# Optimization experiments

Measured on AMD Instinct MI355X. Metric: run time of the kernel, lower is better.

## Reference

```python
import jax, jax.numpy as jnp
import numpy as np

MS = 0.001
TAU = 50.0
THRESHOLD = 1.0


def setup_inputs() -> dict:
    key = jax.random.key(0)
    kx, kw = jax.random.split(key)
    x = jax.random.normal(kx, (32, 1024, 1000), dtype=jnp.float32)
    # nn.init.normal_(w, mean=0.0, std=8000)
    w = jax.random.normal(kw, (1024, 1024), dtype=jnp.float32) * 8000.0
    return {"x": x, "w": w}


def reference(x, w):
    # x: [B, n_in, T], w: [n_in, n_out]
    # Precompute all input currents in one batched GEMM: [T, B, n_out]
    currents = jnp.einsum('bit,io->tbo', x, w)

    def step(v, cur):
        v = v + (-v + cur) * (MS / TAU)
        spikes = (v >= THRESHOLD).astype(v.dtype)
        v = v * (1.0 - spikes)
        return v, spikes

    v0 = jnp.zeros((x.shape[0], w.shape[1]), dtype=x.dtype)
    _, out = jax.lax.scan(step, v0, currents)  # out: [T, B, n_out]
    return jnp.transpose(out, (1, 2, 0))  # [B, n_out, T]
```

## Files before the change

kernel.cpp:

```cpp
#include <hip/hip_runtime.h>


#define NB 32
#define NI 1024
#define NO 1024
#define NT 1000
#define NS 5
#define BT 64
#define BO 64
#define KI 32
#define NKB (NI/KI)
#define TILEB (NS*2*64*16)

typedef int i32x4  __attribute__((ext_vector_type(4)));
typedef int i32x16 __attribute__((ext_vector_type(16)));

typedef const __attribute__((address_space(1))) void GVOID;
typedef __attribute__((address_space(3))) void LVOID;
#define GLDS16(g, l) __builtin_amdgcn_global_load_lds((GVOID*)(g), (LVOID*)(l), 16, 0, 0)

__global__ void snn_wscale(const float* __restrict__ w, float* __restrict__ sb)
{
    __shared__ float red[4][64];
    const int tid = threadIdx.x;
    const int ol = tid & 63, iq = tid >> 6;
    const int o = blockIdx.x * 64 + ol;
    float m = 0.f;
    for (int i = iq; i < NI; i += 4) m = fmaxf(m, fabsf(w[(size_t)i * NO + o]));
    red[iq][ol] = m;
    __syncthreads();
    if (iq == 0) {
        m = fmaxf(fmaxf(red[0][ol], red[1][ol]), fmaxf(red[2][ol], red[3][ol]));
        const int e = (__float_as_uint(m) >> 23) & 255;
        float S = 0.f, Si = 0.f;
        if (e) {
            S  = __uint_as_float((unsigned)(e + 1) << 23);
            Si = __uint_as_float((unsigned)(253 - e) << 23);
        }
        sb[o] = S;
        sb[NO + o] = Si;
    }
}

__global__ void snn_wslice(const float* __restrict__ w, const float* __restrict__ sb,
                           signed char* __restrict__ wp)
{
    __shared__ int sldw[NS][64][16];
    const int tid = threadIdx.x;
    const int ol = tid & 63, iq = tid >> 6;
    const int o0 = blockIdx.x * 64, ic = blockIdx.y * 64;
    const float inv = sb[NO + o0 + ol];
#pragma unroll
    for (int q4 = 0; q4 < 16; q4 += 4) {
        int pk[NS] = {0, 0, 0, 0, 0};
#pragma unroll
        for (int j = 0; j < 4; ++j) {
            const int i = ic + iq * 16 + q4 + j;
            float wv = w[(size_t)i * NO + o0 + ol] * inv;
#pragma unroll
            for (int s = 0; s < NS; ++s) {
                const float f = wv * 128.f;
                const int a = (int)f;
                wv = f - (float)a;
                pk[s] |= (a & 255) << (8 * j);
            }
        }
        const int cdw = (iq * 16 + q4) >> 2;
#pragma unroll
        for (int s = 0; s < NS; ++s) sldw[s][ol][cdw ^ (ol & 15)] = pk[s];
    }
    __syncthreads();
    signed char* tb = wp + (size_t)blockIdx.x * (NKB * TILEB) + (size_t)(ic >> 5) * TILEB;
#pragma unroll
    for (int p = 0; p < 20; ++p) {
        const int idx = p * 256 + tid;
        const int kbi = idx >= 2560;
        const int ld  = idx - (kbi ? 2560 : 0);
        const int s  = ld >> 9;
        const int kc = (ld >> 8) & 1;
        const int r  = (ld >> 2) & 63;
        const int d4 = ld & 3;
        *(int*)&tb[(size_t)kbi * TILEB + (size_t)ld * 4] =
            sldw[s][r][(kbi * 8 + kc * 4 + d4) ^ (r & 15)];
    }
}

__global__ void snn_xscale(const float* __restrict__ x, float* __restrict__ sa,
                           int t0, int tca)
{
    __shared__ float red[4][64];
    const int tid = threadIdx.x;
    const int tl = tid & 63, iq = tid >> 6;
    const int b = blockIdx.y;
    const int tt = blockIdx.x * 64;
    const int tg = t0 + tt + tl;
    const float* xb = x + (size_t)b * NI * NT;
    float m = 0.f;
    if (tg < NT)
        for (int i = iq; i < NI; i += 4) m = fmaxf(m, fabsf(xb[(size_t)i * NT + tg]));
    red[iq][tl] = m;
    __syncthreads();
    if (iq == 0) {
        m = fmaxf(fmaxf(red[0][tl], red[1][tl]), fmaxf(red[2][tl], red[3][tl]));
        const int e = (__float_as_uint(m) >> 23) & 255;
        sa[(size_t)b * tca + tt + tl] = e ? __uint_as_float((unsigned)(e + 1) << 23) : 0.f;
    }
}

__global__ void snn_xslice(const float* __restrict__ x, const float* __restrict__ sa,
                           signed char* __restrict__ xp, int t0, int tca, int ntiles)
{
    __shared__ int sldw[NS][64][16];
    const int tid = threadIdx.x;
    const int tl = tid & 63, iq = tid >> 6;
    const int b = blockIdx.y;
    const int tile = blockIdx.x;
    const int tg = t0 + tile * 64 + tl;
    const bool valid = (tg < NT);
    const float* xb = x + (size_t)b * NI * NT;
    const float S = sa[(size_t)b * tca + tile * 64 + tl];
    const float inv = (S > 0.f)
        ? __uint_as_float((254u - (__float_as_uint(S) >> 23)) << 23) : 0.f;
    signed char* tb = xp + (size_t)(b * ntiles + tile) * (NKB * TILEB);

    for (int c4 = 0; c4 < 4; ++c4) {
        const int ic = blockIdx.z * 256 + c4 * 64;
#pragma unroll
        for (int q4 = 0; q4 < 16; q4 += 4) {
            int pk[NS] = {0, 0, 0, 0, 0};
#pragma unroll
            for (int j = 0; j < 4; ++j) {
                const int i = ic + iq * 16 + q4 + j;
                float wv = valid ? xb[(size_t)i * NT + tg] * inv : 0.f;
#pragma unroll
                for (int s = 0; s < NS; ++s) {
                    const float f = wv * 128.f;
                    const int a = (int)f;
                    wv = f - (float)a;
                    pk[s] |= (a & 255) << (8 * j);
                }
            }
            const int cdw = (iq * 16 + q4) >> 2;
#pragma unroll
            for (int s = 0; s < NS; ++s) sldw[s][tl][cdw ^ (tl & 15)] = pk[s];
        }
        __syncthreads();
        signed char* kbb = tb + (size_t)(ic >> 5) * TILEB;
#pragma unroll
        for (int p = 0; p < 20; ++p) {
            const int idx = p * 256 + tid;
            const int kbi = idx >= 2560;
            const int ld  = idx - (kbi ? 2560 : 0);
            const int s  = ld >> 9;
            const int kc = (ld >> 8) & 1;
            const int r  = (ld >> 2) & 63;
            const int d4 = ld & 3;
            *(int*)&kbb[(size_t)kbi * TILEB + (size_t)ld * 4] =
                sldw[s][r][(kbi * 8 + kc * 4 + d4) ^ (r & 15)];
        }
        __syncthreads();
    }
}

__global__ __launch_bounds__(256, 4)
void snn_gemm_i8(const signed char* __restrict__ xp, const signed char* __restrict__ wp,
                 const float* __restrict__ sa, const float* __restrict__ sb,
                 double* __restrict__ cur, int t0, int tca, int ntiles)
{
    __shared__ signed char As[2][TILEB];
    __shared__ signed char Bs[2][TILEB];

    const int tid  = threadIdx.x;
    const int lane = tid & 63;
    const int wave = tid >> 6;
    const int wm = (wave >> 1) * 32;
    const int wn = (wave & 1) * 32;
    const int l31 = lane & 31;
    const int hi  = lane >> 5;

    int lid = blockIdx.x + (int)gridDim.x * (blockIdx.y + (int)gridDim.y * blockIdx.z);
    {
        const int nwg = (int)(gridDim.x * gridDim.y * gridDim.z);
        const int q = nwg >> 3, r = nwg & 7;
        const int xcd = lid & 7, off = lid >> 3;
        lid = (xcd < r ? xcd * (q + 1) : r * (q + 1) + (xcd - r) * q) + off;
    }
    const int ox  = lid & 15;
    const int rst = lid >> 4;
    const int ty  = rst % ntiles;
    const int b   = rst / ntiles;

    const int o0 = ox * BO;
    const int bt = ty * BT;

    i32x16 acc[NS];
#pragma unroll
    for (int c = 0; c < NS; ++c) acc[c] = (i32x16)0;

    const signed char* AgL = xp + (size_t)(b * ntiles + ty) * (NKB * TILEB) + lane * 16;
    const signed char* BgL = wp + (size_t)ox * (NKB * TILEB) + lane * 16;

#define STAGE(src, bsel) do {                                                  \
    if (wave < 2) {                                                            \
        _Pragma("unroll")                                                      \
        for (int u = 0; u < 5; ++u) {                                          \
            const int ck = wave * 5 + u;                                       \
            GLDS16(AgL + (size_t)(src) * TILEB + ck * 1024,                    \
                   &As[bsel][0] + ck * 1024);                                  \
        }                                                                      \
    } else {                                                                   \
        _Pragma("unroll")                                                      \
        for (int u = 0; u < 5; ++u) {                                          \
            const int ck = (wave - 2) * 5 + u;                                 \
            GLDS16(BgL + (size_t)(src) * TILEB + ck * 1024,                    \
                   &Bs[bsel][0] + ck * 1024);                                  \
        }                                                                      \
    } } while (0)

    const int abase = hi * 1024 + (wm + l31) * 16;
    const int bbase = hi * 1024 + (wn + l31) * 16;

#define KITER(slot) do {                                                       \
    const signed char* Ab_ = &As[slot][0];                                     \
    const signed char* Bb_ = &Bs[slot][0];                                     \
    i32x4 bf[NS];                                                              \
    _Pragma("unroll")                                                          \
    for (int s = 0; s < NS; ++s) bf[s] = *(const i32x4*)&Bb_[bbase + s * 2048];\
    i32x4 a0 = *(const i32x4*)&Ab_[abase];                                     \
    _Pragma("unroll")                                                          \
    for (int i = 0; i < NS; ++i) {                                             \
        i32x4 a1 = a0;                                                         \
        if (i + 1 < NS) a1 = *(const i32x4*)&Ab_[abase + (i + 1) * 2048];      \
        __builtin_amdgcn_s_setprio(1);                                         \
        _Pragma("unroll")                                                      \
        for (int c = NS - 1; c >= i; --c)                                      \
            acc[c] = __builtin_amdgcn_mfma_i32_32x32x32_i8(a0, bf[c - i],      \
                                                           acc[c], 0, 0, 0);   \
        __builtin_amdgcn_s_setprio(0);                                         \
        a0 = a1;                                                               \
    } } while (0)

    STAGE(0, 0);
    asm volatile("s_waitcnt vmcnt(0)" ::: "memory");
    __builtin_amdgcn_s_barrier();

    for (int kb = 0; kb < NKB - 1; ++kb) {
        STAGE(kb + 1, (kb + 1) & 1);
        KITER(kb & 1);
        asm volatile("s_waitcnt vmcnt(0)" ::: "memory");
        asm volatile("s_waitcnt lgkmcnt(0)" ::: "memory");
        __builtin_amdgcn_sched_barrier(0);
        __builtin_amdgcn_s_barrier();
    }
    KITER((NKB - 1) & 1);
#undef STAGE
#undef KITER

    int prow[16];
    {
        i32x4 pa, pb;
#pragma unroll
        for (int q = 0; q < 4; ++q) {
            int va = 0, vb = 0;
#pragma unroll
            for (int jj = 0; jj < 4; ++jj) {
                const int k = 16 * hi + q * 4 + jj;
                if (l31 == k) va |= 1 << (8 * jj);
                vb |= (k & 255) << (8 * jj);
            }
            pa[q] = va; pb[q] = vb;
        }
        i32x16 pp = (i32x16)0;
        pp = __builtin_amdgcn_mfma_i32_32x32x32_i8(pa, pb, pp, 0, 0, 0);
#pragma unroll
        for (int r = 0; r < 16; ++r) prow[r] = pp[r] & 31;
    }

    const double c128[NS] = {0x1p-14, 0x1p-21, 0x1p-28, 0x1p-35, 0x1p-42};
    const int ocol = o0 + wn + l31;
    const double sbv = (double)sb[ocol];
#pragma unroll
    for (int r = 0; r < 16; ++r) {
        const int trow = bt + wm + prow[r];
        double v = 0.0;
#pragma unroll
        for (int c = 0; c < NS; ++c) v += (double)acc[c][r] * c128[c];
        v *= (double)sa[(size_t)b * tca + trow] * sbv;
        if (t0 + trow < NT)
            cur[((size_t)trow * NB + b) * NO + ocol] = v;
    }
}

#define NC 32
__global__ __launch_bounds__(64)
void snn_scan_f64(const double* __restrict__ cur, float* __restrict__ out,
                  double* __restrict__ vstate, int t0, int len)
{
    const int gid = blockIdx.x * 64 + threadIdx.x;
    const double dt = 0.001 / 50.0;

    double v = (t0 == 0) ? 0.0 : vstate[gid];
    const double* cp = cur + gid;
    float* op = out + (size_t)gid * NT + t0;

    const size_t ts = (size_t)NB * NO;
    const int nb = len / NC;
    const int rem = len - nb * NC;

    double A[NC], B[NC];
#pragma unroll
    for (int j = 0; j < NC; ++j) A[j] = (j < len) ? cp[(size_t)j * ts] : 0.0;

    for (int blk = 0; blk < nb; ++blk) {
        const int next = (blk + 1) * NC;
#pragma unroll
        for (int j = 0; j < NC; ++j)
            B[j] = (next + j < len) ? cp[(size_t)(next + j) * ts] : 0.0;

#pragma unroll
        for (int q = 0; q < NC; q += 8) {
            float s[8];
#pragma unroll
            for (int j = 0; j < 8; ++j) {
                v = v + (A[q + j] - v) * dt;
                const bool sp = (v >= 1.0);
                s[j] = sp ? 1.0f : 0.0f;
                if (sp) v = 0.0;
            }
            *(float4*)(op + q)     = make_float4(s[0], s[1], s[2], s[3]);
            *(float4*)(op + q + 4) = make_float4(s[4], s[5], s[6], s[7]);
        }
        op += NC;
#pragma unroll
        for (int j = 0; j < NC; ++j) A[j] = B[j];
    }

    for (int q = 0; q < rem; q += 8) {
        float s[8];
#pragma unroll
        for (int j = 0; j < 8; ++j) {
            v = v + (A[q + j] - v) * dt;
            const bool sp = (v >= 1.0);
            s[j] = sp ? 1.0f : 0.0f;
            if (sp) v = 0.0;
        }
        *(float4*)(op + q)     = make_float4(s[0], s[1], s[2], s[3]);
        *(float4*)(op + q + 4) = make_float4(s[4], s[5], s[6], s[7]);
    }
    vstate[gid] = v;
}

extern "C" void kernel_launch(void* const* d_in, const int* in_sizes, int n_in,
                              void* d_out, int out_size, void* d_ws, size_t ws_size,
                              hipStream_t stream)
{
    const float* x = (const float*)d_in[0];
    const float* w = (const float*)d_in[1];
    float* out = (float*)d_out;

    char* p = (char*)d_ws;
    double* vstate = (double*)p;         p += (size_t)NB * NO * 8;
    float* sbv = (float*)p;              p += (size_t)2 * NO * 4;
    signed char* wp = (signed char*)p;   p += (size_t)(NO / 64) * NKB * TILEB;

    const size_t fixed = (size_t)(p - (char*)d_ws);
    const size_t per_t = (size_t)NB * 4
                       + (size_t)NS * NB * NI
                       + (size_t)NB * NO * 8;
    int tca = 512;
    while (tca > 64 && fixed + (size_t)tca * per_t > ws_size) tca -= 64;

    float* sa = (float*)p;               p += (size_t)NB * tca * 4;
    signed char* xpl = (signed char*)p;  p += (size_t)NB * (tca / 64) * NKB * TILEB;
    double* cur = (double*)p;

    snn_wscale<<<dim3(NO / 64), dim3(256), 0, stream>>>(w, sbv);
    snn_wslice<<<dim3(NO / 64, NI / 64), dim3(256), 0, stream>>>(w, sbv, wp);

    for (int t0 = 0; t0 < NT; t0 += tca) {
        const int len = (NT - t0 < tca) ? (NT - t0) : tca;
        const int ntiles = (len + BT - 1) / BT;
        snn_xscale<<<dim3(ntiles, NB), dim3(256), 0, stream>>>(x, sa, t0, tca);
        snn_xslice<<<dim3(ntiles, NB, 4), dim3(256), 0, stream>>>(x, sa, xpl, t0, tca, ntiles);
        snn_gemm_i8<<<dim3(NO / BO, ntiles, NB), dim3(256), 0, stream>>>(
            xpl, wp, sa, sbv, cur, t0, tca, ntiles);
        snn_scan_f64<<<dim3((NB * NO) / 64), dim3(64), 0, stream>>>(
            cur, out, vstate, t0, len);
    }
}
```

Measured before the change: 1.061 ms.

## Load A fragments directly to registers and triple-buffer B in LDS

The int8 GEMM no longer stages the A tile through shared memory. Each wave loads its A fragments from global memory straight into registers, using two alternating register sets. B stays in LDS, now with three buffers and a counted vmcnt wait, so loads can run further ahead of the MFMA work. This removes the LDS traffic and space for A and deepens the pipeline, but it costs more VGPRs, which is why launch bounds drop to 3 waves per SIMD, and the A global loads are duplicated across waves.

Result: no change. 1.072 ms (+1.1%).

```diff
diff --git a/kernel.cpp b/kernel.cpp
--- a/kernel.cpp
+++ b/kernel.cpp
@@ -162,13 +162,12 @@
     }
 }
 
-__global__ __launch_bounds__(256, 4)
+__global__ __launch_bounds__(256, 3)
 void snn_gemm_i8(const signed char* __restrict__ xp, const signed char* __restrict__ wp,
                  const float* __restrict__ sa, const float* __restrict__ sb,
                  double* __restrict__ cur, int t0, int tca, int ntiles)
 {
-    __shared__ signed char As[2][TILEB];
-    __shared__ signed char Bs[2][TILEB];
+    __shared__ signed char Bs[3][TILEB];
 
     const int tid  = threadIdx.x;
     const int lane = tid & 63;
@@ -197,64 +196,69 @@
 #pragma unroll
     for (int c = 0; c < NS; ++c) acc[c] = (i32x16)0;
 
-    const signed char* AgL = xp + (size_t)(b * ntiles + ty) * (NKB * TILEB) + lane * 16;
-    const signed char* BgL = wp + (size_t)ox * (NKB * TILEB) + lane * 16;
-
-#define STAGE(src, bsel) do {                                                  \
-    if (wave < 2) {                                                            \
-        _Pragma("unroll")                                                      \
-        for (int u = 0; u < 5; ++u) {                                          \
-            const int ck = wave * 5 + u;                                       \
-            GLDS16(AgL + (size_t)(src) * TILEB + ck * 1024,                    \
-                   &As[bsel][0] + ck * 1024);                                  \
-        }                                                                      \
-    } else {                                                                   \
-        _Pragma("unroll")                                                      \
-        for (int u = 0; u < 5; ++u) {                                          \
-            const int ck = (wave - 2) * 5 + u;                                 \
-            GLDS16(BgL + (size_t)(src) * TILEB + ck * 1024,                    \
-                   &Bs[bsel][0] + ck * 1024);                                  \
-        }                                                                      \
+    const signed char* Ag = xp + (size_t)(b * ntiles + ty) * (NKB * TILEB)
+                               + hi * 1024 + (wm + l31) * 16;
+    const signed char* Bg = wp + (size_t)ox * (NKB * TILEB) + lane * 16;
+    const int bbase = hi * 1024 + (wn + l31) * 16;
+
+#define ISSUE(src, aset, slot) do {                                            \
+    const signed char* As_ = Ag + (size_t)(src) * TILEB;                       \
+    _Pragma("unroll")                                                          \
+    for (int s = 0; s < NS; ++s)                                               \
+        aset[s] = *(const i32x4*)(As_ + s * 2048);                             \
+    const signed char* Bsrc_ = Bg + (size_t)(src) * TILEB;                     \
+    _Pragma("unroll")                                                          \
+    for (int u = 0; u < 3; ++u) {                                              \
+        int ck = 3 * wave + u; if (ck >= 10) ck -= 10;                         \
+        GLDS16(Bsrc_ + ck * 1024, &Bs[slot][0] + ck * 1024);                   \
     } } while (0)
 
-    const int abase = hi * 1024 + (wm + l31) * 16;
-    const int bbase = hi * 1024 + (wn + l31) * 16;
-
-#define KITER(slot) do {                                                       \
-    const signed char* Ab_ = &As[slot][0];                                     \
+#define COMPUTE(aset, slot) do {                                               \
     const signed char* Bb_ = &Bs[slot][0];                                     \
-    i32x4 bf[NS];                                                              \
+    i32x4 bcur = *(const i32x4*)&Bb_[bbase];                                   \
     _Pragma("unroll")                                                          \
-    for (int s = 0; s < NS; ++s) bf[s] = *(const i32x4*)&Bb_[bbase + s * 2048];\
-    i32x4 a0 = *(const i32x4*)&Ab_[abase];                                     \
-    _Pragma("unroll")                                                          \
-    for (int i = 0; i < NS; ++i) {                                             \
-        i32x4 a1 = a0;                                                         \
-        if (i + 1 < NS) a1 = *(const i32x4*)&Ab_[abase + (i + 1) * 2048];      \
+    for (int j = 0; j < NS; ++j) {                                             \
+        i32x4 bnext = bcur;                                                    \
+        if (j + 1 < NS) bnext = *(const i32x4*)&Bb_[bbase + (j + 1) * 2048];   \
         __builtin_amdgcn_s_setprio(1);                                         \
         _Pragma("unroll")                                                      \
-        for (int c = NS - 1; c >= i; --c)                                      \
-            acc[c] = __builtin_amdgcn_mfma_i32_32x32x32_i8(a0, bf[c - i],      \
-                                                           acc[c], 0, 0, 0);   \
+        for (int i = 0; i + j < NS; ++i)                                       \
+            acc[i + j] = __builtin_amdgcn_mfma_i32_32x32x32_i8(                \
+                aset[i], bcur, acc[i + j], 0, 0, 0);                           \
         __builtin_amdgcn_s_setprio(0);                                         \
-        a0 = a1;                                                               \
+        bcur = bnext;                                                          \
     } } while (0)
 
-    STAGE(0, 0);
-    asm volatile("s_waitcnt vmcnt(0)" ::: "memory");
-    __builtin_amdgcn_s_barrier();
-
-    for (int kb = 0; kb < NKB - 1; ++kb) {
-        STAGE(kb + 1, (kb + 1) & 1);
-        KITER(kb & 1);
-        asm volatile("s_waitcnt vmcnt(0)" ::: "memory");
-        asm volatile("s_waitcnt lgkmcnt(0)" ::: "memory");
+    i32x4 aE[NS], aO[NS];
+
+    ISSUE(0, aE, 0);
+    __builtin_amdgcn_sched_barrier(0);
+
+    int sl_w = 1;
+    int sl_r = 0;
+    for (int kb = 0; kb < NKB; kb += 2) {
+        ISSUE(kb + 1, aO, sl_w);
+        sl_w = (sl_w == 2) ? 0 : sl_w + 1;
         __builtin_amdgcn_sched_barrier(0);
+        asm volatile("s_waitcnt vmcnt(8)" ::: "memory");
         __builtin_amdgcn_s_barrier();
-    }
-    KITER((NKB - 1) & 1);
-#undef STAGE
-#undef KITER
+        COMPUTE(aE, sl_r);
+        sl_r = (sl_r == 2) ? 0 : sl_r + 1;
+
+        if (kb + 2 < NKB) {
+            ISSUE(kb + 2, aE, sl_w);
+            sl_w = (sl_w == 2) ? 0 : sl_w + 1;
+            __builtin_amdgcn_sched_barrier(0);
+            asm volatile("s_waitcnt vmcnt(8)" ::: "memory");
+        } else {
+            asm volatile("s_waitcnt vmcnt(0)" ::: "memory");
+        }
+        __builtin_amdgcn_s_barrier();
+        COMPUTE(aO, sl_r);
+        sl_r = (sl_r == 2) ? 0 : sl_r + 1;
+    }
+#undef ISSUE
+#undef COMPUTE
 
     int prow[16];
     {
```

## Widen int8 GEMM output tile to 128 columns with per-wave 32x64 register tiles

Applied to the files above, without the earlier changes.

The int8 sliced GEMM block tile grows from 64x64 to 64x128 outputs. Each wave now holds two 32x32 accumulator sets, reusing its A fragments across two B column groups. The weight packing layout is changed to match, and all four waves now share the global-to-LDS staging. This halves A-tile reloads per output and raises MFMA work per LDS read, at the cost of doubled accumulator registers and lower occupancy (launch bounds drop to 2 blocks per CU) plus half as many workgroups.

After: 1.040 ms. No clear change (-1.9%).

```diff
diff --git a/kernel.cpp b/kernel.cpp
--- a/kernel.cpp
+++ b/kernel.cpp
@@ -7,10 +7,11 @@
 #define NT 1000
 #define NS 5
 #define BT 64
-#define BO 64
+#define BO 128
 #define KI 32
 #define NKB (NI/KI)
 #define TILEB (NS*2*64*16)
+#define B_TILEB (NS*2*128*16)
 
 typedef int i32x4  __attribute__((ext_vector_type(4)));
 typedef int i32x16 __attribute__((ext_vector_type(16)));
@@ -70,7 +71,9 @@
         for (int s = 0; s < NS; ++s) sldw[s][ol][cdw ^ (ol & 15)] = pk[s];
     }
     __syncthreads();
-    signed char* tb = wp + (size_t)blockIdx.x * (NKB * TILEB) + (size_t)(ic >> 5) * TILEB;
+    const int o64 = o0 & 64;
+    signed char* tb = wp + (size_t)(o0 >> 7) * (NKB * B_TILEB)
+                         + (size_t)(ic >> 5) * B_TILEB;
 #pragma unroll
     for (int p = 0; p < 20; ++p) {
         const int idx = p * 256 + tid;
@@ -80,7 +83,8 @@
         const int kc = (ld >> 8) & 1;
         const int r  = (ld >> 2) & 63;
         const int d4 = ld & 3;
-        *(int*)&tb[(size_t)kbi * TILEB + (size_t)ld * 4] =
+        const int dofs = (s * 2 + kc) * 512 + (o64 + r) * 4 + d4;
+        *(int*)&tb[(size_t)kbi * B_TILEB + (size_t)dofs * 4] =
             sldw[s][r][(kbi * 8 + kc * 4 + d4) ^ (r & 15)];
     }
 }
@@ -162,19 +166,19 @@
     }
 }
 
-__global__ __launch_bounds__(256, 4)
+__global__ __launch_bounds__(256, 2)
 void snn_gemm_i8(const signed char* __restrict__ xp, const signed char* __restrict__ wp,
                  const float* __restrict__ sa, const float* __restrict__ sb,
                  double* __restrict__ cur, int t0, int tca, int ntiles)
 {
     __shared__ signed char As[2][TILEB];
-    __shared__ signed char Bs[2][TILEB];
+    __shared__ signed char Bs[2][B_TILEB];
 
     const int tid  = threadIdx.x;
     const int lane = tid & 63;
     const int wave = tid >> 6;
     const int wm = (wave >> 1) * 32;
-    const int wn = (wave & 1) * 32;
+    const int wnb = (wave & 1) * 64;
     const int l31 = lane & 31;
     const int hi  = lane >> 5;
 
@@ -185,59 +189,60 @@
         const int xcd = lid & 7, off = lid >> 3;
         lid = (xcd < r ? xcd * (q + 1) : r * (q + 1) + (xcd - r) * q) + off;
     }
-    const int ox  = lid & 15;
-    const int rst = lid >> 4;
+    const int ox  = lid & 7;
+    const int rst = lid >> 3;
     const int ty  = rst % ntiles;
     const int b   = rst / ntiles;
 
     const int o0 = ox * BO;
     const int bt = ty * BT;
 
-    i32x16 acc[NS];
-#pragma unroll
-    for (int c = 0; c < NS; ++c) acc[c] = (i32x16)0;
-
-    const signed char* AgL = xp + (size_t)(b * ntiles + ty) * (NKB * TILEB) + lane * 16;
-    const signed char* BgL = wp + (size_t)ox * (NKB * TILEB) + lane * 16;
+    i32x16 acc[2][NS];
+#pragma unroll
+    for (int ot = 0; ot < 2; ++ot)
+#pragma unroll
+        for (int c = 0; c < NS; ++c) acc[ot][c] = (i32x16)0;
+
+    const signed char* AgD = xp + (size_t)(b * ntiles + ty) * (NKB * TILEB) + lane * 16;
+    const signed char* BgD = wp + (size_t)ox * (NKB * B_TILEB) + lane * 16;
+    const int abase  = hi * 1024 + (wm + l31) * 16;
+    const int bbase0 = hi * 2048 + (wnb + l31) * 16;
+    const int bbase1 = bbase0 + 512;
 
 #define STAGE(src, bsel) do {                                                  \
-    if (wave < 2) {                                                            \
-        _Pragma("unroll")                                                      \
-        for (int u = 0; u < 5; ++u) {                                          \
-            const int ck = wave * 5 + u;                                       \
-            GLDS16(AgL + (size_t)(src) * TILEB + ck * 1024,                    \
-                   &As[bsel][0] + ck * 1024);                                  \
-        }                                                                      \
-    } else {                                                                   \
-        _Pragma("unroll")                                                      \
-        for (int u = 0; u < 5; ++u) {                                          \
-            const int ck = (wave - 2) * 5 + u;                                 \
-            GLDS16(BgL + (size_t)(src) * TILEB + ck * 1024,                    \
-                   &Bs[bsel][0] + ck * 1024);                                  \
-        }                                                                      \
+    _Pragma("unroll")                                                          \
+    for (int u = 0; u < 8; ++u) {                                              \
+        int ck = wave * 8 + u; if (ck >= 30) ck -= 30;                         \
+        const signed char* g = (ck < 10)                                       \
+            ? AgD + (size_t)(src) * TILEB + ck * 1024                          \
+            : BgD + (size_t)(src) * B_TILEB + (ck - 10) * 1024;                \
+        signed char* l = (ck < 10) ? &As[bsel][0] + ck * 1024                  \
+                                   : &Bs[bsel][0] + (ck - 10) * 1024;          \
+        GLDS16(g, l);                                                          \
     } } while (0)
 
-    const int abase = hi * 1024 + (wm + l31) * 16;
-    const int bbase = hi * 1024 + (wn + l31) * 16;
-
-#define KITER(slot) do {                                                       \
+#define COMPUTE(slot) do {                                                     \
     const signed char* Ab_ = &As[slot][0];                                     \
     const signed char* Bb_ = &Bs[slot][0];                                     \
-    i32x4 bf[NS];                                                              \
+    i32x4 af[NS];                                                              \
     _Pragma("unroll")                                                          \
-    for (int s = 0; s < NS; ++s) bf[s] = *(const i32x4*)&Bb_[bbase + s * 2048];\
-    i32x4 a0 = *(const i32x4*)&Ab_[abase];                                     \
+    for (int s = 0; s < NS; ++s)                                               \
+        af[s] = *(const i32x4*)&Ab_[abase + s * 2048];                         \
+    i32x4 bcur = *(const i32x4*)&Bb_[bbase0];                                  \
     _Pragma("unroll")                                                          \
-    for (int i = 0; i < NS; ++i) {                                             \
-        i32x4 a1 = a0;                                                         \
-        if (i + 1 < NS) a1 = *(const i32x4*)&Ab_[abase + (i + 1) * 2048];      \
+    for (int q = 0; q < 10; ++q) {                                             \
+        const int ot = q / 5, j = q % 5;                                       \
+        i32x4 bnext = bcur;                                                    \
+        if (q + 1 < 10)                                                        \
+            bnext = *(const i32x4*)&Bb_[((q + 1) / 5 ? bbase1 : bbase0)        \
+                                        + ((q + 1) % 5) * 4096];               \
         __builtin_amdgcn_s_setprio(1);                                         \
         _Pragma("unroll")                                                      \
-        for (int c = NS - 1; c >= i; --c)                                      \
-            acc[c] = __builtin_amdgcn_mfma_i32_32x32x32_i8(a0, bf[c - i],      \
-                                                           acc[c], 0, 0, 0);   \
+        for (int i = 0; i + j < NS; ++i)                                       \
+            acc[ot][i + j] = __builtin_amdgcn_mfma_i32_32x32x32_i8(            \
+                af[i], bcur, acc[ot][i + j], 0, 0, 0);                         \
         __builtin_amdgcn_s_setprio(0);                                         \
-        a0 = a1;                                                               \
+        bcur = bnext;                                                          \
     } } while (0)
 
     STAGE(0, 0);
@@ -246,15 +251,15 @@
 
     for (int kb = 0; kb < NKB - 1; ++kb) {
         STAGE(kb + 1, (kb + 1) & 1);
-        KITER(kb & 1);
+        COMPUTE(kb & 1);
         asm volatile("s_waitcnt vmcnt(0)" ::: "memory");
         asm volatile("s_waitcnt lgkmcnt(0)" ::: "memory");
         __builtin_amdgcn_sched_barrier(0);
         __builtin_amdgcn_s_barrier();
     }
-    KITER((NKB - 1) & 1);
+    COMPUTE((NKB - 1) & 1);
 #undef STAGE
-#undef KITER
+#undef COMPUTE
 
     int prow[16];
     {
@@ -277,17 +282,20 @@
     }
 
     const double c128[NS] = {0x1p-14, 0x1p-21, 0x1p-28, 0x1p-35, 0x1p-42};
-    const int ocol = o0 + wn + l31;
-    const double sbv = (double)sb[ocol];
-#pragma unroll
-    for (int r = 0; r < 16; ++r) {
-        const int trow = bt + wm + prow[r];
-        double v = 0.0;
-#pragma unroll
-        for (int c = 0; c < NS; ++c) v += (double)acc[c][r] * c128[c];
-        v *= (double)sa[(size_t)b * tca + trow] * sbv;
-        if (t0 + trow < NT)
-            cur[((size_t)trow * NB + b) * NO + ocol] = v;
+#pragma unroll
+    for (int ot = 0; ot < 2; ++ot) {
+        const int ocol = o0 + wnb + ot * 32 + l31;
+        const double sbv = (double)sb[ocol];
+#pragma unroll
+        for (int r = 0; r < 16; ++r) {
+            const int trow = bt + wm + prow[r];
+            double v = 0.0;
+#pragma unroll
+            for (int c = 0; c < NS; ++c) v += (double)acc[ot][c][r] * c128[c];
+            v *= (double)sa[(size_t)b * tca + trow] * sbv;
+            if (t0 + trow < NT)
+                cur[((size_t)trow * NB + b) * NO + ocol] = v;
+        }
     }
 }
 
@@ -361,7 +369,7 @@
     char* p = (char*)d_ws;
     double* vstate = (double*)p;         p += (size_t)NB * NO * 8;
     float* sbv = (float*)p;              p += (size_t)2 * NO * 4;
-    signed char* wp = (signed char*)p;   p += (size_t)(NO / 64) * NKB * TILEB;
+    signed char* wp = (signed char*)p;   p += (size_t)(NO / BO) * NKB * B_TILEB;
 
     const size_t fixed = (size_t)(p - (char*)d_ws);
     const size_t per_t = (size_t)NB * 4
```
